# Performance work log

Hardware: AMD Instinct MI355X
Metric: run time of the kernel (lower is better)

## Reference

```python
import jax, jax.numpy as jnp
import numpy as np

K_HOPS = 3  # spektral TAGConv default
BN_EPS = 1e-3  # keras BatchNormalization default epsilon


def _propagate(x, edge_src, edge_dst, edge_weight, n_nodes):
    # y[dst] += w * x[src]  (sparse adjacency @ x)
    msg = x[edge_src] * edge_weight[:, None]
    return jax.ops.segment_sum(msg, edge_dst, num_segments=n_nodes)


def _tag_conv(x, edge_src, edge_dst, edge_weight, W, b):
    n = x.shape[0]
    hops = [x]
    h = x
    for _ in range(K_HOPS):
        h = _propagate(h, edge_src, edge_dst, edge_weight, n)
        hops.append(h)
    # concat hops along features then dense combine: [N, F*(K+1)] @ [F*(K+1), C]
    return jnp.concatenate(hops, axis=-1) @ W + b


def setup_inputs() -> dict:
    key = jax.random.key(0)
    ks = jax.random.split(key, 6)
    N, F, E, H, L = 20000, 2000, 640000, 128, 15
    x = jax.random.normal(ks[0], (N, F), dtype=jnp.float32)
    edge_src = jax.random.randint(ks[1], (E,), 0, N, dtype=jnp.int32)
    edge_dst = jax.random.randint(ks[2], (E,), 0, N, dtype=jnp.int32)
    # normalized adjacency weights, roughly 1/avg_degree scale
    edge_weight = jax.random.uniform(ks[3], (E,), dtype=jnp.float32) / 32.0
    W1 = jax.random.normal(ks[4], (F * (K_HOPS + 1), H), dtype=jnp.float32) * (1.0 / np.sqrt(F * (K_HOPS + 1)))
    b1 = jnp.zeros((H,), dtype=jnp.float32)
    gamma = jnp.ones((H,), dtype=jnp.float32)
    beta = jnp.zeros((H,), dtype=jnp.float32)
    moving_mean = jnp.zeros((H,), dtype=jnp.float32)
    moving_var = jnp.ones((H,), dtype=jnp.float32)
    W2 = jax.random.normal(ks[5], (H * (K_HOPS + 1), L), dtype=jnp.float32) * (1.0 / np.sqrt(H * (K_HOPS + 1)))
    b2 = jnp.zeros((L,), dtype=jnp.float32)
    return {"x": x, "edge_src": edge_src, "edge_dst": edge_dst, "edge_weight": edge_weight,
            "W1": W1, "b1": b1, "gamma": gamma, "beta": beta,
            "moving_mean": moving_mean, "moving_var": moving_var, "W2": W2, "b2": b2}


def reference(x, edge_src, edge_dst, edge_weight, W1, b1, gamma, beta,
              moving_mean, moving_var, W2, b2):
    # training=False: Dropout is identity, BN uses moving statistics
    h = _tag_conv(x, edge_src, edge_dst, edge_weight, W1, b1)
    h = (h - moving_mean) * jax.lax.rsqrt(moving_var + BN_EPS) * gamma + beta
    h = jax.nn.relu(h)
    z = _tag_conv(h, edge_src, edge_dst, edge_weight, W2, b2)
    return z
```

## Files before the change

kernel.cpp:

```cpp
#include <hip/hip_runtime.h>
#include <hip/hip_bf16.h>
#include <cstdint>
#include <cstddef>

#define N_NODES 20000
#define F_IN    2000
#define H_DIM   128
#define L_DIM   15
#define K_PAD   2048
#define N1      512
#define BM      128
#define BN      128
#define BK      32
#define I_TILES 157

typedef __attribute__((ext_vector_type(4))) float f32x4;
typedef __attribute__((ext_vector_type(8))) short s16x8;
typedef __attribute__((ext_vector_type(8))) unsigned short u16x8;
typedef __attribute__((ext_vector_type(4))) unsigned int u32x4;

__device__ __forceinline__ unsigned short f2bf(float f) {
  unsigned int u = __float_as_uint(f);
  u += 0x7fff + ((u >> 16) & 1);
  return (unsigned short)(u >> 16);
}

__device__ __forceinline__ unsigned int pkbf(float a, float b) {
  union { __hip_bfloat162 h; unsigned int u; } cv;
  cv.h = __float22bfloat162_rn(make_float2(a, b));
  return cv.u;
}

__device__ __forceinline__ float2 bf2f(unsigned int u) {
  float2 r;
  r.x = __uint_as_float(u << 16);
  r.y = __uint_as_float(u & 0xffff0000u);
  return r;
}

__global__ __launch_bounds__(256) void k_cvt_w1(const float* __restrict__ W1,
                                                unsigned short* __restrict__ bt) {
  __shared__ unsigned short tile[128 * 67];
  const int hop = blockIdx.x >> 5;
  const int k0  = (blockIdx.x & 31) * 64;
  const int t = threadIdx.x;
#pragma unroll
  for (int it = 0; it < 8; ++it) {
    int f4 = it * 256 + t;
    int r  = f4 >> 5;
    int c4 = f4 & 31;
    int k = k0 + r;
    float4 v = make_float4(0.f, 0.f, 0.f, 0.f);
    if (k < F_IN) v = *(const float4*)(W1 + (size_t)(hop * F_IN + k) * H_DIM + c4 * 4);
    tile[(c4 * 4 + 0) * 67 + r] = f2bf(v.x);
    tile[(c4 * 4 + 1) * 67 + r] = f2bf(v.y);
    tile[(c4 * 4 + 2) * 67 + r] = f2bf(v.z);
    tile[(c4 * 4 + 3) * 67 + r] = f2bf(v.w);
  }
  __syncthreads();
  const int c = t >> 1, kh = (t & 1) * 32;
  unsigned short* dst = bt + (size_t)(hop * 128 + c) * K_PAD + k0 + kh;
  const unsigned short* srcp = tile + c * 67 + kh;
#pragma unroll
  for (int q = 0; q < 4; ++q) {
    u16x8 o;
#pragma unroll
    for (int e = 0; e < 8; ++e) o[e] = srcp[q * 8 + e];
    *(u16x8*)(dst + q * 8) = o;
  }
}

__global__ __launch_bounds__(256) void k_gemm1(const float* __restrict__ X,
                                               const unsigned short* __restrict__ B,
                                               float* __restrict__ C0,
                                               float* __restrict__ C1) {
  __shared__ unsigned short As[BM * BK];
  __shared__ unsigned short Bs[BN * BK];
  const int b = blockIdx.x;
  const int i_tile = (b & 7) + 8 * (b >> 6);
  const int mid = (b >> 3) & 7;
  const int j_tile = mid & 3;
  const int ks = mid >> 2;
  if (i_tile >= I_TILES) return;
  const int rowA0 = i_tile * BM;
  const int colB0 = j_tile * BN;
  const int tid  = threadIdx.x;
  const int lane = tid & 63;
  const int wave = tid >> 6;
  const int wm = (wave >> 1) * 64;
  const int wn = (wave & 1) * 64;
  const int quad = lane >> 4;
  const int l15  = lane & 15;
  f32x4 acc[4][4] = {};

  const int kend = ks ? F_IN : 1024;
  for (int kt = ks * 1024; kt < kend; kt += BK) {
#pragma unroll
    for (int r = 0; r < 2; ++r) {
      int c = r * 256 + tid;
      int row = c >> 2;
      int kc = (c & 3) * 8;
      const unsigned short* gb = B + (size_t)(colB0 + row) * K_PAD + kt + kc;
      __builtin_amdgcn_global_load_lds((const __attribute__((address_space(1))) void*)gb,
                                       (__attribute__((address_space(3))) void*)(Bs + c * 8),
                                       16, 0, 0);
    }
#pragma unroll
    for (int r = 0; r < 2; ++r) {
      int c = r * 256 + tid;
      int row = c >> 2;
      int kc = (c & 3) * 8;
      int grow = rowA0 + row;
      int gk = kt + kc;
      float4 va = make_float4(0.f, 0.f, 0.f, 0.f);
      float4 vb = make_float4(0.f, 0.f, 0.f, 0.f);
      if (grow < N_NODES && gk < F_IN) {
        const float* p = X + (size_t)grow * F_IN + gk;
        va = *(const float4*)p;
        vb = *(const float4*)(p + 4);
      }
      u32x4 w;
      w.x = pkbf(va.x, va.y); w.y = pkbf(va.z, va.w);
      w.z = pkbf(vb.x, vb.y); w.w = pkbf(vb.z, vb.w);
      *(u32x4*)(As + (size_t)c * 8) = w;
    }
    __syncthreads();
    s16x8 af[4], bfr[4];
#pragma unroll
    for (int i = 0; i < 4; ++i)
      af[i] = *(const s16x8*)(As + (wm + i * 16 + l15) * BK + quad * 8);
#pragma unroll
    for (int j = 0; j < 4; ++j)
      bfr[j] = *(const s16x8*)(Bs + (wn + j * 16 + l15) * BK + quad * 8);
#pragma unroll
    for (int i = 0; i < 4; ++i)
#pragma unroll
      for (int j = 0; j < 4; ++j)
        acc[i][j] = __builtin_amdgcn_mfma_f32_16x16x32_bf16(af[i], bfr[j], acc[i][j], 0, 0, 0);
    __syncthreads();
  }

  float* Cp = ks ? C1 : C0;
#pragma unroll
  for (int i = 0; i < 4; ++i) {
    int row0 = rowA0 + wm + i * 16 + quad * 4;
#pragma unroll
    for (int j = 0; j < 4; ++j) {
      int col = colB0 + wn + j * 16 + l15;
#pragma unroll
      for (int r = 0; r < 4; ++r) {
        int row = row0 + r;
        if (row < N_NODES) Cp[(size_t)row * N1 + col] = acc[i][j][r];
      }
    }
  }
}

__global__ __launch_bounds__(256) void k_comb(float* __restrict__ C0,
                                              const float* __restrict__ C1,
                                              unsigned short* __restrict__ Yb3) {
  unsigned int t = blockIdx.x * 256u + threadIdx.x;
  unsigned int row = t >> 7;
  unsigned int c4 = (t & 127u) * 4u;
  size_t idx = (size_t)row * N1 + c4;
  float4 a = *(const float4*)(C0 + idx);
  float4 b = *(const float4*)(C1 + idx);
  float4 s = make_float4(a.x + b.x, a.y + b.y, a.z + b.z, a.w + b.w);
  if (c4 < 384) {
    *(float4*)(C0 + idx) = s;
  } else {
    unsigned int u0 = pkbf(s.x, s.y), u1 = pkbf(s.z, s.w);
    *(uint2*)(Yb3 + (size_t)row * H_DIM + (c4 - 384)) = make_uint2(u0, u1);
  }
}

__global__ __launch_bounds__(256) void k_hist(const int* __restrict__ dst,
                                              int* __restrict__ deg, int E) {
  int i = blockIdx.x * 256 + threadIdx.x;
  int e = i * 4;
  if (e + 4 <= E) {
    int4 d4 = *(const int4*)(dst + e);
    atomicAdd(&deg[d4.x], 1); atomicAdd(&deg[d4.y], 1);
    atomicAdd(&deg[d4.z], 1); atomicAdd(&deg[d4.w], 1);
  } else {
    for (; e < E; ++e) atomicAdd(&deg[dst[e]], 1);
  }
}

__global__ __launch_bounds__(1024) void k_scan(const int* __restrict__ deg,
                                               int* __restrict__ rowStart,
                                               int* __restrict__ cursor) {
  __shared__ int sums[1024];
  const int t = threadIdx.x;
  const int chunk = (N_NODES + 1023) / 1024;
  int lo = t * chunk;
  int hi = lo + chunk; if (hi > N_NODES) hi = N_NODES;
  int s = 0;
  for (int i = lo; i < hi; ++i) s += deg[i];
  sums[t] = s;
  __syncthreads();
  for (int off = 1; off < 1024; off <<= 1) {
    int v = sums[t];
    int u = (t >= off) ? sums[t - off] : 0;
    __syncthreads();
    sums[t] = v + u;
    __syncthreads();
  }
  int run = sums[t] - s;
  for (int i = lo; i < hi; ++i) {
    rowStart[i] = run; cursor[i] = run; run += deg[i];
  }
  if (t == 1023) rowStart[N_NODES] = run;
}

__global__ __launch_bounds__(256) void k_scatter(const int* __restrict__ src,
                                                 const int* __restrict__ dst,
                                                 const float* __restrict__ w,
                                                 int* cursor,
                                                 int2* __restrict__ eSW, int E) {
  int e = blockIdx.x * 256 + threadIdx.x;
  if (e >= E) return;
  int p = atomicAdd(&cursor[dst[e]], 1);
  eSW[p] = make_int2(src[e], __float_as_int(w[e]));
}

__global__ __launch_bounds__(256) void k_prop128b(const int* __restrict__ rowStart,
    const int2* __restrict__ eSW,
    const unsigned short* __restrict__ gsrc,
    const float* __restrict__ addv, int addStride, int addOff,
    unsigned short* __restrict__ outb, float* __restrict__ outf,
    const float* __restrict__ b1, const float* __restrict__ gamma,
    const float* __restrict__ beta, const float* __restrict__ mean,
    const float* __restrict__ var, int doBN) {
  const int lane = threadIdx.x & 63;
  const int d = blockIdx.x * 4 + (threadIdx.x >> 6);
  const int s0 = rowStart[d], s1 = rowStart[d + 1];
  const int c2 = lane * 2;
  float ax = 0.f, ay = 0.f;
  int j = s0;
  for (; j + 8 <= s1; j += 8) {
    int2 e0 = eSW[j],     e1 = eSW[j + 1], e2 = eSW[j + 2], e3 = eSW[j + 3];
    int2 e4 = eSW[j + 4], e5 = eSW[j + 5], e6 = eSW[j + 6], e7 = eSW[j + 7];
    unsigned int g0 = *(const unsigned int*)(gsrc + (size_t)e0.x * H_DIM + c2);
    unsigned int g1 = *(const unsigned int*)(gsrc + (size_t)e1.x * H_DIM + c2);
    unsigned int g2 = *(const unsigned int*)(gsrc + (size_t)e2.x * H_DIM + c2);
    unsigned int g3 = *(const unsigned int*)(gsrc + (size_t)e3.x * H_DIM + c2);
    unsigned int g4 = *(const unsigned int*)(gsrc + (size_t)e4.x * H_DIM + c2);
    unsigned int g5 = *(const unsigned int*)(gsrc + (size_t)e5.x * H_DIM + c2);
    unsigned int g6 = *(const unsigned int*)(gsrc + (size_t)e6.x * H_DIM + c2);
    unsigned int g7 = *(const unsigned int*)(gsrc + (size_t)e7.x * H_DIM + c2);
    float2 v0 = bf2f(g0), v1 = bf2f(g1), v2 = bf2f(g2), v3 = bf2f(g3);
    float2 v4 = bf2f(g4), v5 = bf2f(g5), v6 = bf2f(g6), v7 = bf2f(g7);
    float w0 = __int_as_float(e0.y), w1 = __int_as_float(e1.y);
    float w2 = __int_as_float(e2.y), w3 = __int_as_float(e3.y);
    float w4 = __int_as_float(e4.y), w5 = __int_as_float(e5.y);
    float w6 = __int_as_float(e6.y), w7 = __int_as_float(e7.y);
    ax = fmaf(w0, v0.x, ax); ay = fmaf(w0, v0.y, ay);
    ax = fmaf(w1, v1.x, ax); ay = fmaf(w1, v1.y, ay);
    ax = fmaf(w2, v2.x, ax); ay = fmaf(w2, v2.y, ay);
    ax = fmaf(w3, v3.x, ax); ay = fmaf(w3, v3.y, ay);
    ax = fmaf(w4, v4.x, ax); ay = fmaf(w4, v4.y, ay);
    ax = fmaf(w5, v5.x, ax); ay = fmaf(w5, v5.y, ay);
    ax = fmaf(w6, v6.x, ax); ay = fmaf(w6, v6.y, ay);
    ax = fmaf(w7, v7.x, ax); ay = fmaf(w7, v7.y, ay);
  }
  for (; j < s1; ++j) {
    int2 e = eSW[j];
    float2 v = bf2f(*(const unsigned int*)(gsrc + (size_t)e.x * H_DIM + c2));
    float w = __int_as_float(e.y);
    ax = fmaf(w, v.x, ax); ay = fmaf(w, v.y, ay);
  }
  float2 av = *(const float2*)(addv + (size_t)d * addStride + addOff + c2);
  float r0 = av.x + ax, r1 = av.y + ay;
  if (doBN) {
    float2 bb = *(const float2*)(b1 + c2);
    float2 gg = *(const float2*)(gamma + c2);
    float2 be = *(const float2*)(beta + c2);
    float2 mm = *(const float2*)(mean + c2);
    float2 vv = *(const float2*)(var + c2);
    r0 = (r0 + bb.x - mm.x) * rsqrtf(vv.x + 1e-3f) * gg.x + be.x;
    r1 = (r1 + bb.y - mm.y) * rsqrtf(vv.y + 1e-3f) * gg.y + be.y;
    r0 = r0 > 0.f ? r0 : 0.f;
    r1 = r1 > 0.f ? r1 : 0.f;
    *(float2*)(outf + (size_t)d * H_DIM + c2) = make_float2(r0, r1);
  } else {
    *(unsigned int*)(outb + (size_t)d * H_DIM + c2) = pkbf(r0, r1);
  }
}

__global__ __launch_bounds__(256) void k_gemm2(const float* __restrict__ Hh,
                                               const float* __restrict__ W2,
                                               float* __restrict__ Y2) {
  __shared__ float w2s[512 * 15];
  for (int i = threadIdx.x; i < 512 * 15; i += 256) w2s[i] = W2[i];
  __syncthreads();
  const int c = threadIdx.x & 63;
  const int d = blockIdx.x * 4 + (threadIdx.x >> 6);
  if (c >= 60 || d >= N_NODES) return;
  const int hop = c / 15, j = c % 15;
  const float4* hr4 = (const float4*)(Hh + (size_t)d * H_DIM);
  float acc = 0.f;
#pragma unroll 8
  for (int k4 = 0; k4 < 32; ++k4) {
    float4 h = hr4[k4];
    const float* wp = w2s + ((hop << 7) + k4 * 4) * 15 + j;
    acc = fmaf(h.x, wp[0],  acc);
    acc = fmaf(h.y, wp[15], acc);
    acc = fmaf(h.z, wp[30], acc);
    acc = fmaf(h.w, wp[45], acc);
  }
  Y2[(size_t)d * 60 + c] = acc;
}

__global__ __launch_bounds__(256) void k_prop15(const int* __restrict__ rowStart,
    const int2* __restrict__ eSW,
    const float* __restrict__ in, int inStride, int inOff,
    const float* __restrict__ addv, int addStride, int addOff,
    const float* __restrict__ bias, float* __restrict__ out) {
  const int f = threadIdx.x & 15;
  const int d = blockIdx.x * 16 + (threadIdx.x >> 4);
  if (f >= 15) return;
  const int s0 = rowStart[d], s1 = rowStart[d + 1];
  float acc = 0.f;
  int j = s0;
  for (; j + 4 <= s1; j += 4) {
    int2 e0 = eSW[j], e1 = eSW[j + 1], e2 = eSW[j + 2], e3 = eSW[j + 3];
    float v0 = in[(size_t)e0.x * inStride + inOff + f];
    float v1 = in[(size_t)e1.x * inStride + inOff + f];
    float v2 = in[(size_t)e2.x * inStride + inOff + f];
    float v3 = in[(size_t)e3.x * inStride + inOff + f];
    acc = fmaf(__int_as_float(e0.y), v0, acc);
    acc = fmaf(__int_as_float(e1.y), v1, acc);
    acc = fmaf(__int_as_float(e2.y), v2, acc);
    acc = fmaf(__int_as_float(e3.y), v3, acc);
  }
  for (; j < s1; ++j) {
    int2 e = eSW[j];
    acc = fmaf(__int_as_float(e.y), in[(size_t)e.x * inStride + inOff + f], acc);
  }
  float b = bias ? bias[f] : 0.f;
  out[(size_t)d * 15 + f] = addv[(size_t)d * addStride + addOff + f] + acc + b;
}

extern "C" void kernel_launch(void* const* d_in, const int* in_sizes, int n_in,
                              void* d_out, int out_size, void* d_ws, size_t ws_size,
                              hipStream_t stream) {
  const float* x     = (const float*)d_in[0];
  const int*   esrc  = (const int*)d_in[1];
  const int*   edst  = (const int*)d_in[2];
  const float* ew    = (const float*)d_in[3];
  const float* W1    = (const float*)d_in[4];
  const float* b1    = (const float*)d_in[5];
  const float* gamma = (const float*)d_in[6];
  const float* beta  = (const float*)d_in[7];
  const float* mmean = (const float*)d_in[8];
  const float* mvar  = (const float*)d_in[9];
  const float* W2    = (const float*)d_in[10];
  const float* b2    = (const float*)d_in[11];
  const int E = in_sizes[1];
  char* ws = (char*)d_ws;

  float*          C0   = (float*)(ws);
  float*          C1   = (float*)(ws + 40960000);
  unsigned short* Yb3  = (unsigned short*)(ws + 81920000);
  unsigned short* w1r  = (unsigned short*)(ws + 87040000);
  int2*           eSW  = (int2*)(ws + 89137152);
  int*            deg      = (int*)(ws + 94257152);
  int*            rowStart = (int*)(ws + 94337280);
  int*            cursor   = (int*)(ws + 94417408);
  unsigned short* P   = (unsigned short*)(ws + 40960000);
  unsigned short* Q   = (unsigned short*)(ws + 46080000);
  float*          Hb  = (float*)(ws + 51200000);
  float*          Y2  = (float*)(ws + 61440000);
  float*          zP  = (float*)(ws + 66240000);
  float*          zQ  = (float*)(ws + 67440000);
  float*          Y   = C0;
  float*          zout = (float*)d_out;

  hipMemsetAsync(deg, 0, N_NODES * sizeof(int), stream);
  k_hist<<<(E / 4 + 255) / 256 + 1, 256, 0, stream>>>(edst, deg, E);
  k_scan<<<1, 1024, 0, stream>>>(deg, rowStart, cursor);
  k_scatter<<<(E + 255) / 256, 256, 0, stream>>>(esrc, edst, ew, cursor, eSW, E);

  k_cvt_w1<<<128, 256, 0, stream>>>(W1, w1r);
  k_gemm1<<<1280, 256, 0, stream>>>(x, w1r, C0, C1);
  k_comb<<<(N_NODES * 128) / 256, 256, 0, stream>>>(C0, C1, Yb3);

  k_prop128b<<<N_NODES / 4, 256, 0, stream>>>(rowStart, eSW, Yb3, Y, N1, 2 * H_DIM,
                                              P, nullptr, b1, gamma, beta, mmean, mvar, 0);
  k_prop128b<<<N_NODES / 4, 256, 0, stream>>>(rowStart, eSW, P, Y, N1, 1 * H_DIM,
                                              Q, nullptr, b1, gamma, beta, mmean, mvar, 0);
  k_prop128b<<<N_NODES / 4, 256, 0, stream>>>(rowStart, eSW, Q, Y, N1, 0,
                                              nullptr, Hb, b1, gamma, beta, mmean, mvar, 1);

  k_gemm2<<<N_NODES / 4, 256, 0, stream>>>(Hb, W2, Y2);
  k_prop15<<<N_NODES / 16, 256, 0, stream>>>(rowStart, eSW, Y2, 60, 45, Y2, 60, 30, nullptr, zP);
  k_prop15<<<N_NODES / 16, 256, 0, stream>>>(rowStart, eSW, zP, 15, 0, Y2, 60, 15, nullptr, zQ);
  k_prop15<<<N_NODES / 16, 256, 0, stream>>>(rowStart, eSW, zQ, 15, 0, Y2, 60, 0, b2, zout);
}
```

Baseline: 641.4 us.

## Pre-convert X to bf16, async-load A tiles, use atomic split-K, split prop edges

A separate pass converts X to padded bf16, so the GEMM can stream A tiles straight into LDS with global_load_lds instead of loading fp32 and converting in registers. The two split-K halves now atomically add into one zeroed output buffer, which removes the second C buffer and the combine kernel; a small kernel extracts the bf16 hop-3 slice. The 128-wide propagation kernel now splits each row's edges across two waves and reduces the halves through shared memory, raising parallelism per row. The cost is an extra full pass over X, a 40 MB memset, and atomic stores in the GEMM epilogue.

```diff
diff --git a/kernel.cpp b/kernel.cpp
--- a/kernel.cpp
+++ b/kernel.cpp
@@ -17,7 +17,6 @@
 typedef __attribute__((ext_vector_type(4))) float f32x4;
 typedef __attribute__((ext_vector_type(8))) short s16x8;
 typedef __attribute__((ext_vector_type(8))) unsigned short u16x8;
-typedef __attribute__((ext_vector_type(4))) unsigned int u32x4;
 
 __device__ __forceinline__ unsigned short f2bf(float f) {
   unsigned int u = __float_as_uint(f);
@@ -36,6 +35,21 @@
   r.x = __uint_as_float(u << 16);
   r.y = __uint_as_float(u & 0xffff0000u);
   return r;
+}
+
+__global__ __launch_bounds__(256) void k_cvt_x(const float* __restrict__ x,
+                                               unsigned short* __restrict__ xb) {
+  unsigned int t = blockIdx.x * 256u + threadIdx.x;
+  unsigned int row = t >> 8;
+  unsigned int colB = (t & 255u) * 8u;
+  u16x8 o = {0, 0, 0, 0, 0, 0, 0, 0};
+  if (colB < F_IN) {
+    const float4 a = *(const float4*)(x + (size_t)row * F_IN + colB);
+    const float4 b = *(const float4*)(x + (size_t)row * F_IN + colB + 4);
+    o[0] = f2bf(a.x); o[1] = f2bf(a.y); o[2] = f2bf(a.z); o[3] = f2bf(a.w);
+    o[4] = f2bf(b.x); o[5] = f2bf(b.y); o[6] = f2bf(b.z); o[7] = f2bf(b.w);
+  }
+  *(u16x8*)(xb + (size_t)t * 8) = o;
 }
 
 __global__ __launch_bounds__(256) void k_cvt_w1(const float* __restrict__ W1,
@@ -70,10 +84,9 @@
   }
 }
 
-__global__ __launch_bounds__(256) void k_gemm1(const float* __restrict__ X,
+__global__ __launch_bounds__(256) void k_gemm1(const unsigned short* __restrict__ A,
                                                const unsigned short* __restrict__ B,
-                                               float* __restrict__ C0,
-                                               float* __restrict__ C1) {
+                                               float* __restrict__ C0) {
   __shared__ unsigned short As[BM * BK];
   __shared__ unsigned short Bs[BN * BK];
   const int b = blockIdx.x;
@@ -100,30 +113,15 @@
       int c = r * 256 + tid;
       int row = c >> 2;
       int kc = (c & 3) * 8;
+      const unsigned short* ga = A + (size_t)(rowA0 + row) * K_PAD + kt + kc;
+      __builtin_amdgcn_global_load_lds((const __attribute__((address_space(1))) void*)ga,
+                                       (__attribute__((address_space(3))) void*)(As + c * 8),
+                                       16, 0, 0);
       const unsigned short* gb = B + (size_t)(colB0 + row) * K_PAD + kt + kc;
       __builtin_amdgcn_global_load_lds((const __attribute__((address_space(1))) void*)gb,
                                        (__attribute__((address_space(3))) void*)(Bs + c * 8),
                                        16, 0, 0);
     }
-#pragma unroll
-    for (int r = 0; r < 2; ++r) {
-      int c = r * 256 + tid;
-      int row = c >> 2;
-      int kc = (c & 3) * 8;
-      int grow = rowA0 + row;
-      int gk = kt + kc;
-      float4 va = make_float4(0.f, 0.f, 0.f, 0.f);
-      float4 vb = make_float4(0.f, 0.f, 0.f, 0.f);
-      if (grow < N_NODES && gk < F_IN) {
-        const float* p = X + (size_t)grow * F_IN + gk;
-        va = *(const float4*)p;
-        vb = *(const float4*)(p + 4);
-      }
-      u32x4 w;
-      w.x = pkbf(va.x, va.y); w.y = pkbf(va.z, va.w);
-      w.z = pkbf(vb.x, vb.y); w.w = pkbf(vb.z, vb.w);
-      *(u32x4*)(As + (size_t)c * 8) = w;
-    }
     __syncthreads();
     s16x8 af[4], bfr[4];
 #pragma unroll
@@ -140,7 +138,6 @@
     __syncthreads();
   }
 
-  float* Cp = ks ? C1 : C0;
 #pragma unroll
   for (int i = 0; i < 4; ++i) {
     int row0 = rowA0 + wm + i * 16 + quad * 4;
@@ -150,28 +147,20 @@
 #pragma unroll
       for (int r = 0; r < 4; ++r) {
         int row = row0 + r;
-        if (row < N_NODES) Cp[(size_t)row * N1 + col] = acc[i][j][r];
+        if (row < N_NODES)
+          unsafeAtomicAdd(&C0[(size_t)row * N1 + col], acc[i][j][r]);
       }
     }
   }
 }
 
-__global__ __launch_bounds__(256) void k_comb(float* __restrict__ C0,
-                                              const float* __restrict__ C1,
-                                              unsigned short* __restrict__ Yb3) {
+__global__ __launch_bounds__(256) void k_mkYb3(const float* __restrict__ C0,
+                                               unsigned short* __restrict__ Yb3) {
   unsigned int t = blockIdx.x * 256u + threadIdx.x;
-  unsigned int row = t >> 7;
-  unsigned int c4 = (t & 127u) * 4u;
-  size_t idx = (size_t)row * N1 + c4;
-  float4 a = *(const float4*)(C0 + idx);
-  float4 b = *(const float4*)(C1 + idx);
-  float4 s = make_float4(a.x + b.x, a.y + b.y, a.z + b.z, a.w + b.w);
-  if (c4 < 384) {
-    *(float4*)(C0 + idx) = s;
-  } else {
-    unsigned int u0 = pkbf(s.x, s.y), u1 = pkbf(s.z, s.w);
-    *(uint2*)(Yb3 + (size_t)row * H_DIM + (c4 - 384)) = make_uint2(u0, u1);
-  }
+  unsigned int row = t >> 5;
+  unsigned int c4 = (t & 31u) * 4u;
+  float4 s = *(const float4*)(C0 + (size_t)row * N1 + 384 + c4);
+  *(uint2*)(Yb3 + (size_t)row * H_DIM + c4) = make_uint2(pkbf(s.x, s.y), pkbf(s.z, s.w));
 }
 
 __global__ __launch_bounds__(256) void k_hist(const int* __restrict__ dst,
@@ -224,7 +213,7 @@
   eSW[p] = make_int2(src[e], __float_as_int(w[e]));
 }
 
-__global__ __launch_bounds__(256) void k_prop128b(const int* __restrict__ rowStart,
+__global__ __launch_bounds__(256) void k_prop128c(const int* __restrict__ rowStart,
     const int2* __restrict__ eSW,
     const unsigned short* __restrict__ gsrc,
     const float* __restrict__ addv, int addStride, int addOff,
@@ -232,44 +221,40 @@
     const float* __restrict__ b1, const float* __restrict__ gamma,
     const float* __restrict__ beta, const float* __restrict__ mean,
     const float* __restrict__ var, int doBN) {
+  __shared__ float red[2][128];
   const int lane = threadIdx.x & 63;
-  const int d = blockIdx.x * 4 + (threadIdx.x >> 6);
+  const int wave = threadIdx.x >> 6;
+  const int rb = wave >> 1;
+  const int h  = wave & 1;
+  const int d = blockIdx.x * 2 + rb;
   const int s0 = rowStart[d], s1 = rowStart[d + 1];
   const int c2 = lane * 2;
   float ax = 0.f, ay = 0.f;
-  int j = s0;
-  for (; j + 8 <= s1; j += 8) {
-    int2 e0 = eSW[j],     e1 = eSW[j + 1], e2 = eSW[j + 2], e3 = eSW[j + 3];
-    int2 e4 = eSW[j + 4], e5 = eSW[j + 5], e6 = eSW[j + 6], e7 = eSW[j + 7];
+  int j = s0 + h;
+  for (; j + 6 < s1; j += 8) {
+    int2 e0 = eSW[j], e1 = eSW[j + 2], e2 = eSW[j + 4], e3 = eSW[j + 6];
     unsigned int g0 = *(const unsigned int*)(gsrc + (size_t)e0.x * H_DIM + c2);
     unsigned int g1 = *(const unsigned int*)(gsrc + (size_t)e1.x * H_DIM + c2);
     unsigned int g2 = *(const unsigned int*)(gsrc + (size_t)e2.x * H_DIM + c2);
     unsigned int g3 = *(const unsigned int*)(gsrc + (size_t)e3.x * H_DIM + c2);
-    unsigned int g4 = *(const unsigned int*)(gsrc + (size_t)e4.x * H_DIM + c2);
-    unsigned int g5 = *(const unsigned int*)(gsrc + (size_t)e5.x * H_DIM + c2);
-    unsigned int g6 = *(const unsigned int*)(gsrc + (size_t)e6.x * H_DIM + c2);
-    unsigned int g7 = *(const unsigned int*)(gsrc + (size_t)e7.x * H_DIM + c2);
     float2 v0 = bf2f(g0), v1 = bf2f(g1), v2 = bf2f(g2), v3 = bf2f(g3);
-    float2 v4 = bf2f(g4), v5 = bf2f(g5), v6 = bf2f(g6), v7 = bf2f(g7);
     float w0 = __int_as_float(e0.y), w1 = __int_as_float(e1.y);
     float w2 = __int_as_float(e2.y), w3 = __int_as_float(e3.y);
-    float w4 = __int_as_float(e4.y), w5 = __int_as_float(e5.y);
-    float w6 = __int_as_float(e6.y), w7 = __int_as_float(e7.y);
     ax = fmaf(w0, v0.x, ax); ay = fmaf(w0, v0.y, ay);
     ax = fmaf(w1, v1.x, ax); ay = fmaf(w1, v1.y, ay);
     ax = fmaf(w2, v2.x, ax); ay = fmaf(w2, v2.y, ay);
     ax = fmaf(w3, v3.x, ax); ay = fmaf(w3, v3.y, ay);
-    ax = fmaf(w4, v4.x, ax); ay = fmaf(w4, v4.y, ay);
-    ax = fmaf(w5, v5.x, ax); ay = fmaf(w5, v5.y, ay);
-    ax = fmaf(w6, v6.x, ax); ay = fmaf(w6, v6.y, ay);
-    ax = fmaf(w7, v7.x, ax); ay = fmaf(w7, v7.y, ay);
-  }
-  for (; j < s1; ++j) {
+  }
+  for (; j < s1; j += 2) {
     int2 e = eSW[j];
     float2 v = bf2f(*(const unsigned int*)(gsrc + (size_t)e.x * H_DIM + c2));
     float w = __int_as_float(e.y);
     ax = fmaf(w, v.x, ax); ay = fmaf(w, v.y, ay);
   }
+  if (h) { red[rb][c2] = ax; red[rb][c2 + 1] = ay; }
+  __syncthreads();
+  if (h) return;
+  ax += red[rb][c2]; ay += red[rb][c2 + 1];
   float2 av = *(const float2*)(addv + (size_t)d * addStride + addOff + c2);
   float r0 = av.x + ax, r1 = av.y + ay;
   if (doBN) {
@@ -360,37 +345,40 @@
   const int E = in_sizes[1];
   char* ws = (char*)d_ws;
 
-  float*          C0   = (float*)(ws);
-  float*          C1   = (float*)(ws + 40960000);
-  unsigned short* Yb3  = (unsigned short*)(ws + 81920000);
-  unsigned short* w1r  = (unsigned short*)(ws + 87040000);
-  int2*           eSW  = (int2*)(ws + 89137152);
-  int*            deg      = (int*)(ws + 94257152);
-  int*            rowStart = (int*)(ws + 94337280);
-  int*            cursor   = (int*)(ws + 94417408);
-  unsigned short* P   = (unsigned short*)(ws + 40960000);
-  unsigned short* Q   = (unsigned short*)(ws + 46080000);
-  float*          Hb  = (float*)(ws + 51200000);
-  float*          Y2  = (float*)(ws + 61440000);
-  float*          zP  = (float*)(ws + 66240000);
-  float*          zQ  = (float*)(ws + 67440000);
+  unsigned short* xb  = (unsigned short*)(ws);
+  float*          C0  = (float*)(ws + 81920000);
+  unsigned short* w1r = (unsigned short*)(ws + 122880000);
+  int2*           eSW = (int2*)(ws + 124977152);
+  int*       deg      = (int*)(ws + 130097152);
+  int*       rowStart = (int*)(ws + 130177280);
+  int*       cursor   = (int*)(ws + 130257408);
+  unsigned short* Yb3 = (unsigned short*)(ws);
+  unsigned short* P   = (unsigned short*)(ws + 5120000);
+  unsigned short* Q   = (unsigned short*)(ws + 10240000);
+  float*          Hb  = (float*)(ws + 15360000);
+  float*          Y2  = (float*)(ws + 25600000);
+  float*          zP  = (float*)(ws + 30400000);
+  float*          zQ  = (float*)(ws + 31600000);
   float*          Y   = C0;
   float*          zout = (float*)d_out;
 
   hipMemsetAsync(deg, 0, N_NODES * sizeof(int), stream);
+  hipMemsetAsync(C0, 0, (size_t)N_NODES * N1 * sizeof(float), stream);
+
   k_hist<<<(E / 4 + 255) / 256 + 1, 256, 0, stream>>>(edst, deg, E);
   k_scan<<<1, 1024, 0, stream>>>(deg, rowStart, cursor);
   k_scatter<<<(E + 255) / 256, 256, 0, stream>>>(esrc, edst, ew, cursor, eSW, E);
 
+  k_cvt_x<<<(N_NODES * K_PAD / 8) / 256, 256, 0, stream>>>(x, xb);
   k_cvt_w1<<<128, 256, 0, stream>>>(W1, w1r);
-  k_gemm1<<<1280, 256, 0, stream>>>(x, w1r, C0, C1);
-  k_comb<<<(N_NODES * 128) / 256, 256, 0, stream>>>(C0, C1, Yb3);
-
-  k_prop128b<<<N_NODES / 4, 256, 0, stream>>>(rowStart, eSW, Yb3, Y, N1, 2 * H_DIM,
+  k_gemm1<<<1280, 256, 0, stream>>>(xb, w1r, C0);
+  k_mkYb3<<<(N_NODES * 32) / 256, 256, 0, stream>>>(C0, Yb3);
+
+  k_prop128c<<<N_NODES / 2, 256, 0, stream>>>(rowStart, eSW, Yb3, Y, N1, 2 * H_DIM,
                                               P, nullptr, b1, gamma, beta, mmean, mvar, 0);
-  k_prop128b<<<N_NODES / 4, 256, 0, stream>>>(rowStart, eSW, P, Y, N1, 1 * H_DIM,
+  k_prop128c<<<N_NODES / 2, 256, 0, stream>>>(rowStart, eSW, P, Y, N1, 1 * H_DIM,
                                               Q, nullptr, b1, gamma, beta, mmean, mvar, 0);
-  k_prop128b<<<N_NODES / 4, 256, 0, stream>>>(rowStart, eSW, Q, Y, N1, 0,
+  k_prop128c<<<N_NODES / 2, 256, 0, stream>>>(rowStart, eSW, Q, Y, N1, 0,
                                               nullptr, Hb, b1, gamma, beta, mmean, mvar, 1);
 
   k_gemm2<<<N_NODES / 4, 256, 0, stream>>>(Hb, W2, Y2);
```

Result: no change. 643.3 us (+0.3%).
